# Kernel tuning notes

Measured on AMD Instinct MI355X. Metric: run time of the kernel, lower is better.

## Reference

```python
import jax, jax.numpy as jnp
import numpy as np

N = 8192          # number of atoms
N_ELEM = 95       # r2r4 table size (elements 0..94)
EPS = 1e-12


def setup_inputs() -> dict:
    key = jax.random.key(0)
    k1, k2, k3 = jax.random.split(key, 3)
    atomic_numbers = jax.random.randint(k1, (N,), 0, N_ELEM)
    # positions in a ~60 Angstrom box so pair distances are realistic
    positions = jax.random.uniform(k2, (N, 3), dtype=jnp.float32) * 60.0
    r2r4 = jax.random.uniform(k3, (N_ELEM,), dtype=jnp.float32)
    # Becke-Johnson damping parameters (PBE D3-BJ)
    a1 = jnp.float32(0.4289)
    a2 = jnp.float32(4.4407)
    s6 = jnp.float32(1.0)
    s8 = jnp.float32(0.7875)
    return {"atomic_numbers": atomic_numbers, "positions": positions,
            "r2r4": r2r4, "a1": a1, "a2": a2, "s6": s6, "s8": s8}


def reference(atomic_numbers, positions, r2r4, a1, a2, s6, s8):
    # Per-atom-type gather (present in source; mathematically unused because
    # the source hard-codes c6 = c8 = 1 via all-ones LazyTensors).
    r2r4_z = r2r4[atomic_numbers]                      # (N,)

    # All-pairs squared distances. d appears only as d^6 and d^8, which are
    # polynomials in d2, so no sqrt is needed (also keeps diagonal smooth).
    diff = positions[:, None, :] - positions[None, :, :]   # (N, N, 3)
    d2 = jnp.sum(diff * diff, axis=-1)                     # (N, N)
    d6 = d2 * d2 * d2
    d8 = d6 * d2

    # c6 = c8 = 1  =>  tmp = a1 * sqrt(c8/c6) + a2 = a1 + a2
    tmp = a1 + a2
    tmp2 = tmp * tmp
    tmp6 = tmp2 * tmp2 * tmp2
    tmp8 = tmp6 * tmp2

    c6 = jnp.float32(1.0)
    c8 = jnp.float32(1.0)
    D_ij = -s6 * c6 / (d6 + tmp6 + EPS) - s8 * c8 / (d8 + tmp8 + EPS)

    # mask d > eps  <=>  d2 > eps^2 (removes self-terms)
    mask = d2 > EPS * EPS
    D_ij = jnp.where(mask, D_ij, jnp.float32(0.0))

    # a_i = sum_j D_ij ; energy = sum_i a_i
    return jnp.sum(D_ij) + jnp.float32(0.0) * jnp.sum(r2r4_z)
```

## Files before the change

### kernel.cpp

```cpp
#include <hip/hip_runtime.h>

#define NA 8192
#define WT 64
#define NTW (NA / WT)
#define NWJOB (NTW * (NTW + 1) / 2)
#define WPB 8
#define BLOCK (WPB * 64)
#define NBLK (NWJOB / WPB)
#define NSLOT 64
#define SLOT_STRIDE 16
#define S_OF(r) ((r) * NTW - (r) * ((r) - 1) / 2)

__device__ __forceinline__ float bcast(float v, int k) {
    return __int_as_float(__builtin_amdgcn_readlane(__float_as_int(v), k));
}

__global__ __launch_bounds__(BLOCK, 8) void dftd3_pair_energy(
    const float* __restrict__ pos,
    const float* __restrict__ p_a1, const float* __restrict__ p_a2,
    const float* __restrict__ p_s6, const float* __restrict__ p_s8,
    float* __restrict__ partial)
{
    const int tid  = threadIdx.x;
    const int lane = tid & 63;
    const int w = __builtin_amdgcn_readfirstlane(blockIdx.x * WPB + (tid >> 6));

    int wi = (int)((2 * NTW + 1 - sqrtf((float)((2 * NTW + 1) * (2 * NTW + 1) - 8 * w))) * 0.5f);
    if (wi > NTW - 1) wi = NTW - 1;
    if (wi < 0) wi = 0;
    while (S_OF(wi + 1) <= w) ++wi;
    while (S_OF(wi) > w) --wi;
    const int wj = wi + (w - S_OF(wi));

    const int i = wi * WT + lane;
    const float xi = pos[3 * i + 0];
    const float yi = pos[3 * i + 1];
    const float zi = pos[3 * i + 2];
    const int j = wj * WT + lane;
    const float vxj = pos[3 * j + 0];
    const float vyj = pos[3 * j + 1];
    const float vzj = pos[3 * j + 2];

    const float a1 = p_a1[0], a2 = p_a2[0];
    const float s6 = p_s6[0], s8 = p_s8[0];
    const float tmp  = a1 + a2;
    const float tmp2 = tmp * tmp;
    const float tmp6 = tmp2 * tmp2 * tmp2;
    const float tmp8 = tmp6 * tmp2;
    const float T6 = tmp6 + 1e-12f;
    const float T8 = tmp8 + 1e-12f;
    const float ns6 = -s6, ns8 = -s8;
    const float EPS2 = 1e-24f;

    float acc0 = 0.0f, acc1 = 0.0f;

    auto body = [&](int k, bool masked) {
        float sx = bcast(vxj, k);
        float sy = bcast(vyj, k);
        float sz = bcast(vzj, k);
        float dx = xi - sx;
        float dy = yi - sy;
        float dz = zi - sz;
        float d2 = fmaf(dx, dx, fmaf(dy, dy, dz * dz));
        float d4 = d2 * d2;
        float d6 = d4 * d2;
        float d8 = d4 * d4;
        float A  = d6 + T6;
        float B  = d8 + T8;
        float num = fmaf(ns6, B, ns8 * A);
        if (masked) num = (d2 > EPS2) ? num : 0.0f;
        float r = __builtin_amdgcn_rcpf(A * B);
        if (k & 1) acc1 = fmaf(num, r, acc1);
        else       acc0 = fmaf(num, r, acc0);
    };

    if (wi == wj) {
        #pragma unroll 8
        for (int k = 0; k < WT; ++k) body(k, true);
    } else {
        #pragma unroll 8
        for (int k = 0; k < WT; ++k) body(k, false);
    }

    float acc = acc0 + acc1;
    if (wi != wj) acc *= 2.0f;

    #pragma unroll
    for (int off = 32; off > 0; off >>= 1)
        acc += __shfl_xor(acc, off, 64);

    __shared__ float wsum[WPB];
    if (lane == 0) wsum[tid >> 6] = acc;
    __syncthreads();
    if (tid == 0) {
        float s = 0.0f;
        #pragma unroll
        for (int q = 0; q < WPB; ++q) s += wsum[q];
        atomicAdd(&partial[(blockIdx.x & (NSLOT - 1)) * SLOT_STRIDE], s);
    }
}

__global__ void reduce_slots(const float* __restrict__ partial, float* __restrict__ out)
{
    if (threadIdx.x == 0) {
        float s = 0.0f;
        #pragma unroll
        for (int k = 0; k < NSLOT; ++k) s += partial[k * SLOT_STRIDE];
        out[0] = s;
    }
}

extern "C" void kernel_launch(void* const* d_in, const int* in_sizes, int n_in,
                              void* d_out, int out_size, void* d_ws, size_t ws_size,
                              hipStream_t stream) {
    const float* pos = (const float*)d_in[1];
    const float* a1  = (const float*)d_in[3];
    const float* a2  = (const float*)d_in[4];
    const float* s6  = (const float*)d_in[5];
    const float* s8  = (const float*)d_in[6];
    float* partial = (float*)d_ws;
    float* out = (float*)d_out;

    hipMemsetAsync(partial, 0, NSLOT * SLOT_STRIDE * sizeof(float), stream);

    dftd3_pair_energy<<<dim3(NBLK), BLOCK, 0, stream>>>(pos, a1, a2, s6, s8, partial);
    reduce_slots<<<1, 64, 0, stream>>>(partial, out);
}
```

Baseline: 94.94 us.

## Pack two i-atoms per lane with shared reciprocal and fuse final reduction

Each lane now handles two i atoms against 64 broadcast j atoms over a 128x64 triangular tiling. The two pair terms share one reciprocal: 1/(den_x*den_y) is computed once and multiplied by the other denominator, with a scale factor to avoid overflow. This roughly halves the rcp instructions and uses packed float2 math. The separate reduce kernel is replaced by a last-block-done reduction using an atomic counter. The risks are precision loss from the scaled denominator product and a different masking scheme on the diagonal tiles.

```diff
diff --git a/kernel.cpp b/kernel.cpp
--- a/kernel.cpp
+++ b/kernel.cpp
@@ -1,45 +1,50 @@
 #include <hip/hip_runtime.h>
 
 #define NA 8192
-#define WT 64
-#define NTW (NA / WT)
-#define NWJOB (NTW * (NTW + 1) / 2)
+#define IT 128
+#define JT 64
+#define NI (NA / IT)
+#define NJ (NA / JT)
+#define NJOB 4160
 #define WPB 8
 #define BLOCK (WPB * 64)
-#define NBLK (NWJOB / WPB)
-#define NSLOT 64
-#define SLOT_STRIDE 16
-#define S_OF(r) ((r) * NTW - (r) * ((r) - 1) / 2)
+#define NBLK (NJOB / WPB)
+#define S_OF(I) ((I) * (129 - (I)))
+
+typedef float v2f __attribute__((ext_vector_type(2)));
 
 __device__ __forceinline__ float bcast(float v, int k) {
     return __int_as_float(__builtin_amdgcn_readlane(__float_as_int(v), k));
 }
 
-__global__ __launch_bounds__(BLOCK, 8) void dftd3_pair_energy(
+__global__ __launch_bounds__(BLOCK, 4) void dftd3_pair_energy(
     const float* __restrict__ pos,
     const float* __restrict__ p_a1, const float* __restrict__ p_a2,
     const float* __restrict__ p_s6, const float* __restrict__ p_s8,
-    float* __restrict__ partial)
+    float* __restrict__ partial, int* __restrict__ cnt,
+    float* __restrict__ out)
 {
     const int tid  = threadIdx.x;
     const int lane = tid & 63;
     const int w = __builtin_amdgcn_readfirstlane(blockIdx.x * WPB + (tid >> 6));
 
-    int wi = (int)((2 * NTW + 1 - sqrtf((float)((2 * NTW + 1) * (2 * NTW + 1) - 8 * w))) * 0.5f);
-    if (wi > NTW - 1) wi = NTW - 1;
-    if (wi < 0) wi = 0;
-    while (S_OF(wi + 1) <= w) ++wi;
-    while (S_OF(wi) > w) --wi;
-    const int wj = wi + (w - S_OF(wi));
+    int I = (int)((129.0f - sqrtf(16641.0f - 4.0f * (float)w)) * 0.5f);
+    if (I < 0) I = 0;
+    if (I > NI - 1) I = NI - 1;
+    while (S_OF(I + 1) <= w) ++I;
+    while (S_OF(I) > w) --I;
+    const int J = 2 * I + (w - S_OF(I));
+    const bool edge = (w - S_OF(I)) < 2;
 
-    const int i = wi * WT + lane;
-    const float xi = pos[3 * i + 0];
-    const float yi = pos[3 * i + 1];
-    const float zi = pos[3 * i + 2];
-    const int j = wj * WT + lane;
+    const int j = J * JT + lane;
     const float vxj = pos[3 * j + 0];
     const float vyj = pos[3 * j + 1];
     const float vzj = pos[3 * j + 2];
+
+    const int i0 = I * IT + 2 * lane;
+    const v2f xi = { pos[3 * i0 + 0], pos[3 * i0 + 3] };
+    const v2f yi = { pos[3 * i0 + 1], pos[3 * i0 + 4] };
+    const v2f zi = { pos[3 * i0 + 2], pos[3 * i0 + 5] };
 
     const float a1 = p_a1[0], a2 = p_a2[0];
     const float s6 = p_s6[0], s8 = p_s8[0];
@@ -49,64 +54,83 @@
     const float tmp8 = tmp6 * tmp2;
     const float T6 = tmp6 + 1e-12f;
     const float T8 = tmp8 + 1e-12f;
-    const float ns6 = -s6, ns8 = -s8;
-    const float EPS2 = 1e-24f;
+    const float SC  = 3.5527137e-15f;
+    const float ns6 = -s6 * SC;
+    const float ns8 = -s8 * SC;
 
-    float acc0 = 0.0f, acc1 = 0.0f;
+    float accx = 0.0f, accy = 0.0f;
 
     auto body = [&](int k, bool masked) {
         float sx = bcast(vxj, k);
         float sy = bcast(vyj, k);
         float sz = bcast(vzj, k);
-        float dx = xi - sx;
-        float dy = yi - sy;
-        float dz = zi - sz;
-        float d2 = fmaf(dx, dx, fmaf(dy, dy, dz * dz));
-        float d4 = d2 * d2;
-        float d6 = d4 * d2;
-        float d8 = d4 * d4;
-        float A  = d6 + T6;
-        float B  = d8 + T8;
-        float num = fmaf(ns6, B, ns8 * A);
-        if (masked) num = (d2 > EPS2) ? num : 0.0f;
-        float r = __builtin_amdgcn_rcpf(A * B);
-        if (k & 1) acc1 = fmaf(num, r, acc1);
-        else       acc0 = fmaf(num, r, acc0);
+        v2f dx = xi - sx;
+        v2f dy = yi - sy;
+        v2f dz = zi - sz;
+        v2f d2 = __builtin_elementwise_fma(dx, dx,
+                 __builtin_elementwise_fma(dy, dy, dz * dz));
+        v2f d4 = d2 * d2;
+        v2f A  = __builtin_elementwise_fma(d4, d2, (v2f)T6);
+        v2f B  = __builtin_elementwise_fma(d4, d4, (v2f)T8);
+        v2f num = __builtin_elementwise_fma((v2f)ns6, B, (v2f)ns8 * A);
+        v2f den = A * B;
+        v2f dens = den * (v2f)SC;
+        float t = dens.x * dens.y;
+        float r = __builtin_amdgcn_rcpf(t);
+        float numx = num.x, numy = num.y;
+        if (masked) {
+            const int jk = J * JT + k;
+            numx = (jk > i0)     ? numx : 0.0f;
+            numy = (jk > i0 + 1) ? numy : 0.0f;
+        }
+        accx = fmaf(numx, dens.y * r, accx);
+        accy = fmaf(numy, dens.x * r, accy);
     };
 
-    if (wi == wj) {
+    if (edge) {
         #pragma unroll 8
-        for (int k = 0; k < WT; ++k) body(k, true);
+        for (int k = 0; k < JT; ++k) body(k, true);
     } else {
         #pragma unroll 8
-        for (int k = 0; k < WT; ++k) body(k, false);
+        for (int k = 0; k < JT; ++k) body(k, false);
     }
 
-    float acc = acc0 + acc1;
-    if (wi != wj) acc *= 2.0f;
+    float acc = 2.0f * (accx + accy);
 
     #pragma unroll
     for (int off = 32; off > 0; off >>= 1)
         acc += __shfl_xor(acc, off, 64);
 
     __shared__ float wsum[WPB];
+    __shared__ int lastflag;
     if (lane == 0) wsum[tid >> 6] = acc;
     __syncthreads();
     if (tid == 0) {
         float s = 0.0f;
         #pragma unroll
         for (int q = 0; q < WPB; ++q) s += wsum[q];
-        atomicAdd(&partial[(blockIdx.x & (NSLOT - 1)) * SLOT_STRIDE], s);
+        atomicExch(&partial[blockIdx.x], s);
+        __threadfence();
+        int old = atomicAdd(cnt, 1);
+        lastflag = (old == NBLK - 1);
     }
-}
-
-__global__ void reduce_slots(const float* __restrict__ partial, float* __restrict__ out)
-{
-    if (threadIdx.x == 0) {
+    __syncthreads();
+    if (lastflag) {
+        __threadfence();
         float s = 0.0f;
+        for (int t = tid; t < NBLK; t += BLOCK)
+            s += atomicAdd(&partial[t], 0.0f);
         #pragma unroll
-        for (int k = 0; k < NSLOT; ++k) s += partial[k * SLOT_STRIDE];
-        out[0] = s;
+        for (int off = 32; off > 0; off >>= 1)
+            s += __shfl_xor(s, off, 64);
+        if (lane == 0) wsum[tid >> 6] = s;
+        __syncthreads();
+        if (tid == 0) {
+            float tot = 0.0f;
+            #pragma unroll
+            for (int q = 0; q < WPB; ++q) tot += wsum[q];
+            out[0] = tot;
+        }
     }
 }
 
@@ -119,10 +143,11 @@
     const float* s6  = (const float*)d_in[5];
     const float* s8  = (const float*)d_in[6];
     float* partial = (float*)d_ws;
-    float* out = (float*)d_out;
+    int*   cnt     = (int*)((char*)d_ws + 65536);
+    float* out     = (float*)d_out;
 
-    hipMemsetAsync(partial, 0, NSLOT * SLOT_STRIDE * sizeof(float), stream);
+    hipMemsetAsync(cnt, 0, sizeof(int), stream);
 
-    dftd3_pair_energy<<<dim3(NBLK), BLOCK, 0, stream>>>(pos, a1, a2, s6, s8, partial);
-    reduce_slots<<<1, 64, 0, stream>>>(partial, out);
+    dftd3_pair_energy<<<dim3(NBLK), BLOCK, 0, stream>>>(pos, a1, a2, s6, s8,
+                                                        partial, cnt, out);
 }
```

Result: faster. 87.50 us (-7.8%).
